# Kernel optimization log

Hardware: AMD Instinct MI355X
Metric: run time of the kernel (lower is better)

Reference implementation:

```python
import jax, jax.numpy as jnp
import numpy as np

B, S, I, H = 1, 4096, 4096, 4096  # batch, seq_len(=input_size), input_size, hidden_size


def setup_inputs() -> dict:
    key = jax.random.key(0)
    ks = jax.random.split(key, 6)
    sc = 1.0 / np.sqrt(H).astype(np.float32)
    x = jax.random.normal(ks[0], (B, I), jnp.float32)
    hidden = jax.random.normal(ks[1], (B, H), jnp.float32)
    # PyTorch GRUCell params, gate order [r, z, n]
    w_ih = jax.random.uniform(ks[2], (3 * H, I), jnp.float32, -sc, sc)
    w_hh = jax.random.uniform(ks[3], (3 * H, H), jnp.float32, -sc, sc)
    b_ih = jax.random.uniform(ks[4], (3 * H,), jnp.float32, -sc, sc)
    b_hh = jax.random.uniform(ks[5], (3 * H,), jnp.float32, -sc, sc)
    return {"x": x, "hidden": hidden, "w_ih": w_ih, "w_hh": w_hh, "b_ih": b_ih, "b_hh": b_hh}


def gru_cell(x, h, w_ih, w_hh, b_ih, b_hh):
    gi = x @ w_ih.T + b_ih  # [B, 3H]
    gh = h @ w_hh.T + b_hh  # [B, 3H]
    i_r, i_z, i_n = jnp.split(gi, 3, axis=-1)
    h_r, h_z, h_n = jnp.split(gh, 3, axis=-1)
    r = jax.nn.sigmoid(i_r + h_r)
    z = jax.nn.sigmoid(i_z + h_z)
    n = jnp.tanh(i_n + r * h_n)
    return (1.0 - z) * h + z * n  # [B, H]


def reference(x, hidden, w_ih, w_hh, b_ih, b_hh):
    seq_len = x.shape[1]
    b = gru_cell(x, hidden, w_ih, w_hh, b_ih, b_hh)  # [B, H]
    a = jax.nn.relu(b)  # relu(b[:, t]) for all t at once

    # out_0 = relu(b[:,0]) + roll(hidden, 1, -1); [B] + [B,H] broadcasts (B==1)
    out0 = a[:, 0] + jnp.roll(hidden, 1, axis=-1)  # [B, H]

    def step(prev, a_t):  # prev: [B, H], a_t: [B]
        out = a_t + jnp.roll(prev, 1, axis=-1)
        return out, out

    _, rest = jax.lax.scan(step, out0, a[:, 1:seq_len].T)  # rest: [S-1, B, H]
    outputs = jnp.concatenate([out0[:, None], jnp.moveaxis(rest, 0, 1)], axis=1)  # [B, S, H]
    new_hidden = outputs[:, -1, :]
    # torch .squeeze(2) is a no-op since H != 1
    return outputs, new_hidden
```

## Files before the change

### kernel.cpp

```cpp
#include <hip/hip_runtime.h>


#define H4 4096
#define R3 12288

__global__ __launch_bounds__(256) void gemv_kernel(
    const float* __restrict__ x,
    const float* __restrict__ hidden,
    const float* __restrict__ w_ih,
    const float* __restrict__ w_hh,
    const float* __restrict__ b_ih,
    const float* __restrict__ b_hh,
    float* __restrict__ g) {
  const int wave = blockIdx.x * 4 + (threadIdx.x >> 6);
  const int lane = threadIdx.x & 63;

  const float* vec;
  const float* wmat;
  const float* bias;
  int row;
  if (wave < R3) { vec = x;      wmat = w_ih; bias = b_ih; row = wave; }
  else           { vec = hidden; wmat = w_hh; bias = b_hh; row = wave - R3; }

  const float4* wrow = reinterpret_cast<const float4*>(wmat + (size_t)row * H4);
  const float4* vv   = reinterpret_cast<const float4*>(vec);

  float ax = 0.f, ay = 0.f, az = 0.f, aw = 0.f;
#pragma unroll
  for (int it = 0; it < 16; ++it) {
    const int idx = it * 64 + lane;
    float4 wq = wrow[idx];
    float4 vq = vv[idx];
    ax = fmaf(wq.x, vq.x, ax);
    ay = fmaf(wq.y, vq.y, ay);
    az = fmaf(wq.z, vq.z, az);
    aw = fmaf(wq.w, vq.w, aw);
  }
  float acc = (ax + ay) + (az + aw);
#pragma unroll
  for (int s = 32; s > 0; s >>= 1) acc += __shfl_down(acc, s, 64);
  if (lane == 0) g[wave] = acc + bias[row];
}

__global__ __launch_bounds__(1024) void combine_scan_kernel(
    const float* __restrict__ hidden,
    const float* __restrict__ g,
    float* __restrict__ prefix,
    float* __restrict__ out_newh) {
  const int tid = threadIdx.x;
  const int s0 = tid * 4;

  float a[4];
#pragma unroll
  for (int k = 0; k < 4; ++k) {
    const int s = s0 + k;
    const float r = 1.f / (1.f + __expf(-(g[s] + g[R3 + s])));
    const float z = 1.f / (1.f + __expf(-(g[H4 + s] + g[R3 + H4 + s])));
    const float n = tanhf(g[2 * H4 + s] + r * g[R3 + 2 * H4 + s]);
    const float h = hidden[s];
    const float b = (1.f - z) * h + z * n;
    a[k] = fmaxf(b, 0.f);
  }
  const float c0 = a[0], c1 = c0 + a[1], c2 = c1 + a[2], c3 = c2 + a[3];
  const float tsum = c3;

  const int lane = tid & 63, wid = tid >> 6;
  float v = tsum;
#pragma unroll
  for (int d = 1; d < 64; d <<= 1) {
    float o = __shfl_up(v, d, 64);
    if (lane >= d) v += o;
  }
  __shared__ float wsum[16];
  if (lane == 63) wsum[wid] = v;
  __syncthreads();
  if (tid < 16) {
    float w = wsum[tid];
#pragma unroll
    for (int d = 1; d < 16; d <<= 1) {
      float o = __shfl_up(w, d, 64);
      if (tid >= d) w += o;
    }
    wsum[tid] = w;
  }
  __syncthreads();

  const float excl = (wid ? wsum[wid - 1] : 0.f) + (v - tsum);
  prefix[s0 + 0] = excl + c0;
  prefix[s0 + 1] = excl + c1;
  prefix[s0 + 2] = excl + c2;
  prefix[s0 + 3] = excl + c3;

  const float total = wsum[15];
#pragma unroll
  for (int k = 0; k < 4; ++k) {
    const int s = s0 + k;
    out_newh[s] = total + hidden[s];
  }
}

__global__ __launch_bounds__(256) void outputs_kernel(
    const float* __restrict__ prefix,
    const float* __restrict__ hidden,
    float* __restrict__ out) {
  const int b = blockIdx.x;
  const int t = b >> 1;
  const int j0 = (b & 1) * 2048 + threadIdx.x * 8;
  const float p = prefix[t];
  const int base = (j0 - t - 1) & 4095;

  float4 o0, o1;
  o0.x = p + hidden[base];
  o0.y = p + hidden[(base + 1) & 4095];
  o0.z = p + hidden[(base + 2) & 4095];
  o0.w = p + hidden[(base + 3) & 4095];
  o1.x = p + hidden[(base + 4) & 4095];
  o1.y = p + hidden[(base + 5) & 4095];
  o1.z = p + hidden[(base + 6) & 4095];
  o1.w = p + hidden[(base + 7) & 4095];

  float* dst = out + (size_t)t * H4 + j0;
  *reinterpret_cast<float4*>(dst)     = o0;
  *reinterpret_cast<float4*>(dst + 4) = o1;
}

extern "C" void kernel_launch(void* const* d_in, const int* in_sizes, int n_in,
                              void* d_out, int out_size, void* d_ws, size_t ws_size,
                              hipStream_t stream) {
  const float* x      = (const float*)d_in[0];
  const float* hidden = (const float*)d_in[1];
  const float* w_ih   = (const float*)d_in[2];
  const float* w_hh   = (const float*)d_in[3];
  const float* b_ih   = (const float*)d_in[4];
  const float* b_hh   = (const float*)d_in[5];
  float* out = (float*)d_out;

  float* ws     = (float*)d_ws;
  float* g      = ws;
  float* prefix = ws + 24576;

  gemv_kernel<<<6144, 256, 0, stream>>>(x, hidden, w_ih, w_hh, b_ih, b_hh, g);
  combine_scan_kernel<<<1, 1024, 0, stream>>>(hidden, g, prefix,
                                              out + (size_t)H4 * H4);
  outputs_kernel<<<8192, 256, 0, stream>>>(prefix, hidden, out);
}
```

Baseline: 444.4 us.

## Compute four GEMV rows per wave with vector staged in shared memory

The GEMV kernel now loads the input vector into LDS once per block, and each wave computes four output rows. The grid shrinks to a quarter of its size. This cuts redundant global vector reads and raises memory-level parallelism per thread, at the cost of fewer resident waves. The combine kernel also switches to float4 loads and stores.

New measurement: 448.8 us. No clear change (+1.0%).

```diff
diff --git a/kernel.cpp b/kernel.cpp
--- a/kernel.cpp
+++ b/kernel.cpp
@@ -12,34 +12,69 @@
     const float* __restrict__ b_ih,
     const float* __restrict__ b_hh,
     float* __restrict__ g) {
-  const int wave = blockIdx.x * 4 + (threadIdx.x >> 6);
+  __shared__ float4 vs[1024];
+
+  const int block = blockIdx.x;
+  const bool isX = (block < 768);
+  const float* vec  = isX ? x    : hidden;
+  const float* wmat = isX ? w_ih : w_hh;
+  const float* bias = isX ? b_ih : b_hh;
+  const int rowb = (isX ? block : block - 768) * 16;
+  const int gbase = isX ? 0 : R3;
+
+  const float4* vv = reinterpret_cast<const float4*>(vec);
+#pragma unroll
+  for (int i = 0; i < 4; ++i) {
+    const int idx = i * 256 + threadIdx.x;
+    vs[idx] = vv[idx];
+  }
+  __syncthreads();
+
+  const int wid = threadIdx.x >> 6;
   const int lane = threadIdx.x & 63;
+  const int row0 = rowb + wid * 4;
+  const float4* w0 = reinterpret_cast<const float4*>(wmat + (size_t)row0 * H4);
 
-  const float* vec;
-  const float* wmat;
-  const float* bias;
-  int row;
-  if (wave < R3) { vec = x;      wmat = w_ih; bias = b_ih; row = wave; }
-  else           { vec = hidden; wmat = w_hh; bias = b_hh; row = wave - R3; }
+  float4 acc0 = {0.f, 0.f, 0.f, 0.f};
+  float4 acc1 = {0.f, 0.f, 0.f, 0.f};
+  float4 acc2 = {0.f, 0.f, 0.f, 0.f};
+  float4 acc3 = {0.f, 0.f, 0.f, 0.f};
 
-  const float4* wrow = reinterpret_cast<const float4*>(wmat + (size_t)row * H4);
-  const float4* vv   = reinterpret_cast<const float4*>(vec);
-
-  float ax = 0.f, ay = 0.f, az = 0.f, aw = 0.f;
 #pragma unroll
   for (int it = 0; it < 16; ++it) {
     const int idx = it * 64 + lane;
-    float4 wq = wrow[idx];
-    float4 vq = vv[idx];
-    ax = fmaf(wq.x, vq.x, ax);
-    ay = fmaf(wq.y, vq.y, ay);
-    az = fmaf(wq.z, vq.z, az);
-    aw = fmaf(wq.w, vq.w, aw);
+    const float4 v4 = vs[idx];
+    const float4 wq0 = w0[idx];
+    const float4 wq1 = w0[1024 + idx];
+    const float4 wq2 = w0[2048 + idx];
+    const float4 wq3 = w0[3072 + idx];
+    acc0.x = fmaf(wq0.x, v4.x, acc0.x); acc0.y = fmaf(wq0.y, v4.y, acc0.y);
+    acc0.z = fmaf(wq0.z, v4.z, acc0.z); acc0.w = fmaf(wq0.w, v4.w, acc0.w);
+    acc1.x = fmaf(wq1.x, v4.x, acc1.x); acc1.y = fmaf(wq1.y, v4.y, acc1.y);
+    acc1.z = fmaf(wq1.z, v4.z, acc1.z); acc1.w = fmaf(wq1.w, v4.w, acc1.w);
+    acc2.x = fmaf(wq2.x, v4.x, acc2.x); acc2.y = fmaf(wq2.y, v4.y, acc2.y);
+    acc2.z = fmaf(wq2.z, v4.z, acc2.z); acc2.w = fmaf(wq2.w, v4.w, acc2.w);
+    acc3.x = fmaf(wq3.x, v4.x, acc3.x); acc3.y = fmaf(wq3.y, v4.y, acc3.y);
+    acc3.z = fmaf(wq3.z, v4.z, acc3.z); acc3.w = fmaf(wq3.w, v4.w, acc3.w);
   }
-  float acc = (ax + ay) + (az + aw);
+
+  float s0 = (acc0.x + acc0.y) + (acc0.z + acc0.w);
+  float s1 = (acc1.x + acc1.y) + (acc1.z + acc1.w);
+  float s2 = (acc2.x + acc2.y) + (acc2.z + acc2.w);
+  float s3 = (acc3.x + acc3.y) + (acc3.z + acc3.w);
 #pragma unroll
-  for (int s = 32; s > 0; s >>= 1) acc += __shfl_down(acc, s, 64);
-  if (lane == 0) g[wave] = acc + bias[row];
+  for (int d = 32; d > 0; d >>= 1) {
+    s0 += __shfl_down(s0, d, 64);
+    s1 += __shfl_down(s1, d, 64);
+    s2 += __shfl_down(s2, d, 64);
+    s3 += __shfl_down(s3, d, 64);
+  }
+  if (lane == 0) {
+    g[gbase + row0 + 0] = s0 + bias[row0 + 0];
+    g[gbase + row0 + 1] = s1 + bias[row0 + 1];
+    g[gbase + row0 + 2] = s2 + bias[row0 + 2];
+    g[gbase + row0 + 3] = s3 + bias[row0 + 3];
+  }
 }
 
 __global__ __launch_bounds__(1024) void combine_scan_kernel(
@@ -50,15 +85,29 @@
   const int tid = threadIdx.x;
   const int s0 = tid * 4;
 
+  const float4 gir = reinterpret_cast<const float4*>(g)[tid];
+  const float4 giz = reinterpret_cast<const float4*>(g + H4)[tid];
+  const float4 gin = reinterpret_cast<const float4*>(g + 2 * H4)[tid];
+  const float4 ghr = reinterpret_cast<const float4*>(g + R3)[tid];
+  const float4 ghz = reinterpret_cast<const float4*>(g + R3 + H4)[tid];
+  const float4 ghn = reinterpret_cast<const float4*>(g + R3 + 2 * H4)[tid];
+  const float4 h4v = reinterpret_cast<const float4*>(hidden)[tid];
+
+  const float ir[4] = {gir.x, gir.y, gir.z, gir.w};
+  const float iz[4] = {giz.x, giz.y, giz.z, giz.w};
+  const float in_[4] = {gin.x, gin.y, gin.z, gin.w};
+  const float hr[4] = {ghr.x, ghr.y, ghr.z, ghr.w};
+  const float hz[4] = {ghz.x, ghz.y, ghz.z, ghz.w};
+  const float hn[4] = {ghn.x, ghn.y, ghn.z, ghn.w};
+  const float hh[4] = {h4v.x, h4v.y, h4v.z, h4v.w};
+
   float a[4];
 #pragma unroll
   for (int k = 0; k < 4; ++k) {
-    const int s = s0 + k;
-    const float r = 1.f / (1.f + __expf(-(g[s] + g[R3 + s])));
-    const float z = 1.f / (1.f + __expf(-(g[H4 + s] + g[R3 + H4 + s])));
-    const float n = tanhf(g[2 * H4 + s] + r * g[R3 + 2 * H4 + s]);
-    const float h = hidden[s];
-    const float b = (1.f - z) * h + z * n;
+    const float r = 1.f / (1.f + __expf(-(ir[k] + hr[k])));
+    const float z = 1.f / (1.f + __expf(-(iz[k] + hz[k])));
+    const float n = tanhf(in_[k] + r * hn[k]);
+    const float b = (1.f - z) * hh[k] + z * n;
     a[k] = fmaxf(b, 0.f);
   }
   const float c0 = a[0], c1 = c0 + a[1], c2 = c1 + a[2], c3 = c2 + a[3];
@@ -86,17 +135,15 @@
   __syncthreads();
 
   const float excl = (wid ? wsum[wid - 1] : 0.f) + (v - tsum);
-  prefix[s0 + 0] = excl + c0;
-  prefix[s0 + 1] = excl + c1;
-  prefix[s0 + 2] = excl + c2;
-  prefix[s0 + 3] = excl + c3;
+  float4 pr;
+  pr.x = excl + c0; pr.y = excl + c1; pr.z = excl + c2; pr.w = excl + c3;
+  reinterpret_cast<float4*>(prefix)[tid] = pr;
 
   const float total = wsum[15];
-#pragma unroll
-  for (int k = 0; k < 4; ++k) {
-    const int s = s0 + k;
-    out_newh[s] = total + hidden[s];
-  }
+  float4 nh;
+  nh.x = total + hh[0]; nh.y = total + hh[1];
+  nh.z = total + hh[2]; nh.w = total + hh[3];
+  reinterpret_cast<float4*>(out_newh)[tid] = nh;
 }
 
 __global__ __launch_bounds__(256) void outputs_kernel(
@@ -139,7 +186,7 @@
   float* g      = ws;
   float* prefix = ws + 24576;
 
-  gemv_kernel<<<6144, 256, 0, stream>>>(x, hidden, w_ih, w_hh, b_ih, b_hh, g);
+  gemv_kernel<<<1536, 256, 0, stream>>>(x, hidden, w_ih, w_hh, b_ih, b_hh, g);
   combine_scan_kernel<<<1, 1024, 0, stream>>>(hidden, g, prefix,
                                               out + (size_t)H4 * H4);
   outputs_kernel<<<8192, 256, 0, stream>>>(prefix, hidden, out);
```
